# Performance work log

Hardware: AMD Instinct MI355X
Metric: run time of the kernel (lower is better)

Reference implementation:

```python
import jax, jax.numpy as jnp
import numpy as np

G = 8  # order of C8 rotation group

def expand_circulant(w):
    # w: [out_fields, in_fields, G] free params of a C8 regular->regular 1x1 conv.
    # Full weight: W[of*G+go, if*G+gi] = w[of, if, (go-gi) mod G]
    g = jnp.arange(G)
    idx = (g[:, None] - g[None, :]) % G            # [go, gi]
    Wf = w[:, :, idx]                              # [of, if, go, gi]
    Wf = jnp.transpose(Wf, (0, 2, 1, 3))           # [of, go, if, gi]
    return Wf.reshape(w.shape[0] * G, w.shape[1] * G)

def eq_proj(x2, w, b):
    # x2: [B, in_fields*G]; equivariant 1x1 conv = GEMM with circulant-expanded weight
    Wf = expand_circulant(w)                       # [out_fields*G, in_fields*G]
    bf = jnp.repeat(b, G)                          # per-field bias, shared across group dim
    return x2 @ Wf.T + bf

def setup_inputs() -> dict:
    key = jax.random.key(0)
    ks = jax.random.split(key, 12)
    B, d_model, n_head, d_k, d_v = 8192, 128, 8, 64, 64
    C = d_model * G                                # 1024
    s_in = 0.02
    inp = {
        'q': jax.random.normal(ks[0], (B, C, 1, 1), jnp.float32),
        'k': jax.random.normal(ks[1], (B, C, 1, 1), jnp.float32),
        'v': jax.random.normal(ks[2], (B, C, 1, 1), jnp.float32),
        'w_q': jax.random.normal(ks[3], (n_head * d_k, d_model, G), jnp.float32) * s_in,
        'b_q': jnp.zeros((n_head * d_k,), jnp.float32),
        'w_k': jax.random.normal(ks[4], (n_head * d_k, d_model, G), jnp.float32) * s_in,
        'b_k': jnp.zeros((n_head * d_k,), jnp.float32),
        'w_v': jax.random.normal(ks[5], (n_head * d_v, d_model, G), jnp.float32) * s_in,
        'b_v': jnp.zeros((n_head * d_v,), jnp.float32),
        'w_fc': jax.random.normal(ks[6], (d_model, n_head * d_v, G), jnp.float32) * s_in,
        'b_fc': jnp.zeros((d_model,), jnp.float32),
    }
    return inp

def reference(q, k, v, w_q, b_q, w_k, b_k, w_v, b_v, w_fc, b_fc):
    B, C = q.shape[0], q.shape[1]
    n_head, d_k = 8, 64
    d_v = 64
    temp = jnp.asarray(d_k ** 0.5, q.dtype)
    residual = q                                   # [B, C, 1, 1]
    q2 = q.reshape(B, C)
    k2 = k.reshape(B, C)
    v2 = v.reshape(B, C)
    # equivariant 1x1 conv projections -> [B, n_head*d_k*G]
    qp = eq_proj(q2, w_q, b_q).reshape(B, G, n_head, d_k).transpose(0, 2, 1, 3)  # [B,H,G,dk]
    kp = eq_proj(k2, w_k, b_k).reshape(B, G, n_head, d_k).transpose(0, 2, 1, 3)
    vp = eq_proj(v2, w_v, b_v).reshape(B, G, n_head, d_v).transpose(0, 2, 1, 3)
    # scaled dot-product attention over the G=8 group/orientation positions
    attn = jax.nn.softmax(jnp.einsum('bhqd,bhkd->bhqk', qp / temp, kp), axis=-1)  # [B,H,G,G]
    out = jnp.einsum('bhqk,bhkd->bhqd', attn, vp)  # [B,H,G,dv]
    # transpose(1,2) then flatten, exactly as torch .view(sz_b, -1, 1, 1)
    out = out.transpose(0, 2, 1, 3).reshape(B, G * n_head * d_v)
    out = eq_proj(out, w_fc, b_fc)                 # [B, d_model*G]
    out = out.reshape(B, C, 1, 1) + residual
    return out, attn
```

## Files before the change

kernel.cpp:

```cpp
#include <hip/hip_runtime.h>
#include <hip/hip_bf16.h>

typedef unsigned short u16;
typedef unsigned int u32;
typedef __bf16 bf16x8_t __attribute__((ext_vector_type(8)));
typedef float f32x4_t __attribute__((ext_vector_type(4)));

#define BK 64

__device__ __forceinline__ float b2f(u16 v) {
  return __uint_as_float(((u32)v) << 16);
}
__device__ __forceinline__ u16 f2b(float f) {
  __hip_bfloat16 h = __float2bfloat16(f);
  return *reinterpret_cast<u16*>(&h);
}
__device__ __forceinline__ float blo(u32 u) { return __uint_as_float(u << 16); }
__device__ __forceinline__ float bhi(u32 u) { return __uint_as_float(u & 0xffff0000u); }

__device__ __forceinline__ void async_lds16(const u16* g, u16* l) {
  __builtin_amdgcn_global_load_lds(
      (__attribute__((address_space(1))) void*)g,
      (__attribute__((address_space(3))) void*)l, 16, 0, 0);
}

__device__ __forceinline__ void expand8(const float* __restrict__ w,
                                        u16* __restrict__ dst, int I,
                                        int kshift, int gid) {
  const int n = gid >> kshift;
  const int kc = (gid & ((1 << kshift) - 1)) * 8;
  const int K = 8 << kshift;
  const float* wp = w + (size_t)((n >> 3) * I + (kc >> 3)) * 8;
  float4 w0 = *(const float4*)wp;
  float4 w1 = *(const float4*)(wp + 4);
  float w8[8] = {w0.x, w0.y, w0.z, w0.w, w1.x, w1.y, w1.z, w1.w};
  u16 t[8];
  const int r = (n - kc) & 7;
#pragma unroll
  for (int j = 0; j < 8; ++j) t[j] = f2b(w8[(r - j) & 7]);
  *(uint4*)(dst + (size_t)n * K + kc) = *(const uint4*)t;
}

__device__ __forceinline__ void cvt8(const float* __restrict__ src,
                                     u16* __restrict__ dst, int gid) {
  const float* p = src + (size_t)gid * 8;
  float4 a = *(const float4*)p;
  float4 b = *(const float4*)(p + 4);
  u16 t[8] = {f2b(a.x), f2b(a.y), f2b(a.z), f2b(a.w),
              f2b(b.x), f2b(b.y), f2b(b.z), f2b(b.w)};
  *(uint4*)(dst + (size_t)gid * 8) = *(const uint4*)t;
}

__global__ __launch_bounds__(256) void expand_all(
    const float* __restrict__ w_q, const float* __restrict__ w_k,
    const float* __restrict__ w_v, const float* __restrict__ w_fc,
    const float* __restrict__ q, const float* __restrict__ k,
    const float* __restrict__ v, u16* __restrict__ Wq, u16* __restrict__ Wk,
    u16* __restrict__ Wv, u16* __restrict__ Wfc, u16* __restrict__ qb,
    u16* __restrict__ kb, u16* __restrict__ vb, int cblocks) {
  const int e = blockIdx.x;
  if (e < 8192) {
    const int plane = e >> 11;
    const int gid = (e & 2047) * 256 + threadIdx.x;
    if (plane == 0) expand8(w_q, Wq, 128, 7, gid);
    else if (plane == 1) expand8(w_k, Wk, 128, 7, gid);
    else if (plane == 2) expand8(w_v, Wv, 128, 7, gid);
    else expand8(w_fc, Wfc, 512, 9, gid);
  } else {
    const int ce = e - 8192;
    const int plane = ce / cblocks;
    const int gid = (ce - plane * cblocks) * 256 + threadIdx.x;
    if (plane == 0) cvt8(q, qb, gid);
    else if (plane == 1) cvt8(k, kb, gid);
    else cvt8(v, vb, gid);
  }
}

__global__ __launch_bounds__(512, 2) void gemm_qkv8p(
    const u16* __restrict__ X0, const u16* __restrict__ X1,
    const u16* __restrict__ X2, const u16* __restrict__ W0,
    const u16* __restrict__ W1, const u16* __restrict__ W2,
    const float* __restrict__ b0v, const float* __restrict__ b1v,
    const float* __restrict__ b2v, u16* __restrict__ Y0, u16* __restrict__ Y1,
    u16* __restrict__ Y2, int M, int N, int K) {
  __shared__ __align__(16) u16 lds[65536];
  const int z = blockIdx.y;
  const u16* X = (z == 0) ? X0 : (z == 1) ? X1 : X2;
  const u16* W = (z == 0) ? W0 : (z == 1) ? W1 : W2;
  const float* bias = (z == 0) ? b0v : (z == 1) ? b1v : b2v;
  u16* Y = (z == 0) ? Y0 : (z == 1) ? Y1 : Y2;

  const int tid = threadIdx.x;
  const int bid = blockIdx.x;
  const int grid_m = M >> 8, grid_n = N >> 8;
  const int nb = grid_m * grid_n;
  int pid = (bid & 7) * (nb >> 3) + (bid >> 3);
  const int nig = 8 * grid_n;
  const int group_id = pid / nig;
  const int first_m = group_id * 8;
  const int gsz = min(8, grid_m - first_m);
  const int mt = first_m + (pid % gsz);
  const int ntile = (pid % nig) / gsz;
  const int m0 = mt << 8, n0 = ntile << 8;

  const int lane = tid & 63, wave = tid >> 6;
  const int wg = wave >> 2;
  const int wq = wave & 3;
  const int l16 = lane & 15, quad = lane >> 4;
  const int lswz = l16 & 7;

  const u16* gA = X + (size_t)m0 * K;
  const u16* gB = W + (size_t)n0 * K;
  const int srow = tid >> 3;
  const int skbg = (tid & 7) ^ (srow & 7);

  f32x4_t acc[8][4] = {};
  const int KT = K >> 6;
  const int niter = KT >> 1;

  auto stg = [&](int kt, int h, bool isB) {
    u16* l = lds + (isB ? 32768 : 0) + ((kt & 1) * 2 + h) * 8192 + tid * 8;
    const u16* g = (isB ? gB : gA) + (size_t)(h * 128 + srow) * K + kt * 64 +
                   skbg * 8;
    async_lds16(g, l);
    async_lds16(g + (size_t)64 * K, l + 4096);
  };
  auto ldA = [&](int kt, int mh, bf16x8_t (&a)[8]) {
    const u16* base = lds + ((kt & 1) * 2 + wg) * 8192 + (mh * 64 + l16) * 64;
#pragma unroll
    for (int mi = 0; mi < 4; ++mi)
#pragma unroll
      for (int ks = 0; ks < 2; ++ks)
        a[mi * 2 + ks] = *(const bf16x8_t*)(base + mi * 1024 +
                                            (((ks * 4 + quad) ^ lswz) * 8));
  };
  auto ldB = [&](int kt, int nh, bf16x8_t (&b)[4]) {
    const u16* base = lds + 32768 + ((kt & 1) * 2 + (wq >> 1)) * 8192 +
                      ((wq & 1) * 64 + nh * 32 + l16) * 64;
#pragma unroll
    for (int ni = 0; ni < 2; ++ni)
#pragma unroll
      for (int ks = 0; ks < 2; ++ks)
        b[ni * 2 + ks] = *(const bf16x8_t*)(base + ni * 1024 +
                                            (((ks * 4 + quad) ^ lswz) * 8));
  };
  auto mm = [&](int mh, int nh, bf16x8_t (&a)[8], bf16x8_t (&b)[4]) {
    __builtin_amdgcn_s_setprio(1);
#pragma unroll
    for (int mi = 0; mi < 4; ++mi)
#pragma unroll
      for (int ni = 0; ni < 2; ++ni)
#pragma unroll
        for (int ks = 0; ks < 2; ++ks)
          acc[mh * 4 + mi][nh * 2 + ni] = __builtin_amdgcn_mfma_f32_16x16x32_bf16(
              a[mi * 2 + ks], b[ni * 2 + ks], acc[mh * 4 + mi][nh * 2 + ni], 0,
              0, 0);
    __builtin_amdgcn_s_setprio(0);
  };
  auto bar = [] { __builtin_amdgcn_s_barrier(); };
  auto lgkm0 = [] {
    asm volatile("s_waitcnt lgkmcnt(0)" ::: "memory");
    __builtin_amdgcn_sched_barrier(0);
  };
  auto sched = [] { __builtin_amdgcn_sched_barrier(0); };

  bf16x8_t a0[8], a1[8], b0[4], b1[4];

  stg(0, 0, false); sched();
  stg(0, 0, true);  sched();
  stg(0, 1, false); sched();
  stg(0, 1, true);  sched();
  stg(1, 0, true);  sched();
  stg(1, 0, false); sched();
  asm volatile("s_waitcnt vmcnt(4)" ::: "memory");
  bar();
  sched();

  for (int it = 0; it < niter; ++it) {
    const int t = it * 2;
    const bool more = (t + 2 < KT);
    ldA(t, 0, a0); ldB(t, 0, b0);
    stg(t + 1, 1, false);
    sched(); bar(); lgkm0();
    mm(0, 0, a0, b0);
    bar();
    ldB(t, 1, b1);
    stg(t + 1, 1, true);
    sched(); bar(); lgkm0();
    mm(0, 1, a0, b1);
    bar();
    ldA(t, 1, a1);
    if (more) stg(t + 2, 0, true);
    sched(); bar(); lgkm0();
    mm(1, 1, a1, b1);
    bar();
    if (more) stg(t + 2, 0, false);
    sched();
    if (more) asm volatile("s_waitcnt vmcnt(4)" ::: "memory");
    else      asm volatile("s_waitcnt vmcnt(0)" ::: "memory");
    bar(); lgkm0();
    mm(1, 0, a1, b0);
    bar();
    ldA(t + 1, 0, a0); ldB(t + 1, 0, b0);
    if (more) stg(t + 2, 1, false);
    sched(); bar(); lgkm0();
    mm(0, 0, a0, b0);
    bar();
    ldB(t + 1, 1, b1);
    if (more) stg(t + 2, 1, true);
    sched(); bar(); lgkm0();
    mm(0, 1, a0, b1);
    bar();
    ldA(t + 1, 1, a1);
    if (more) stg(t + 3, 0, true);
    sched(); bar(); lgkm0();
    mm(1, 1, a1, b1);
    bar();
    if (more) {
      stg(t + 3, 0, false);
      sched();
      asm volatile("s_waitcnt vmcnt(4)" ::: "memory");
      bar(); lgkm0();
      mm(1, 0, a1, b0);
      bar();
    } else {
      lgkm0();
      mm(1, 0, a1, b0);
    }
  }

#pragma unroll
  for (int mi = 0; mi < 8; ++mi) {
#pragma unroll
    for (int r = 0; r < 4; ++r) {
      const int rw = m0 + wg * 128 + mi * 16 + quad * 4 + r;
      u32 h0, h1, h2, h3;
      {
        const int cb = n0 + wq * 64 + l16;
        h0 = (u32)f2b(acc[mi][0][r] + bias[(cb) >> 3]);
        h1 = (u32)f2b(acc[mi][1][r] + bias[(cb + 16) >> 3]);
        h2 = (u32)f2b(acc[mi][2][r] + bias[(cb + 32) >> 3]);
        h3 = (u32)f2b(acc[mi][3][r] + bias[(cb + 48) >> 3]);
      }
      const int s0 = quad * 16 + 4 * (l16 & 3);
      u32 g0[4], g1[4], g2[4], g3[4];
#pragma unroll
      for (int j = 0; j < 4; ++j) {
        g0[j] = (u32)__shfl((int)h0, s0 + j);
        g1[j] = (u32)__shfl((int)h1, s0 + j);
        g2[j] = (u32)__shfl((int)h2, s0 + j);
        g3[j] = (u32)__shfl((int)h3, s0 + j);
      }
      const int myni = l16 >> 2;
      u32 a_[4];
#pragma unroll
      for (int j = 0; j < 4; ++j) {
        u32 s01 = (myni & 1) ? g1[j] : g0[j];
        u32 s23 = (myni & 1) ? g3[j] : g2[j];
        a_[j] = (myni & 2) ? s23 : s01;
      }
      uint2 wv;
      wv.x = a_[0] | (a_[1] << 16);
      wv.y = a_[2] | (a_[3] << 16);
      *(uint2*)&Y[(size_t)rw * N + n0 + wq * 64 + 4 * l16] = wv;
    }
  }
}

__global__ __launch_bounds__(256) void gemm_fc2(
    const u16* __restrict__ Aa, const u16* __restrict__ Ab,
    const u16* __restrict__ W, const float* __restrict__ bias,
    const float* __restrict__ res, float* __restrict__ Y, int M, int N, int K,
    int halfM) {
  constexpr int TN = 128;
  __shared__ __align__(16) u16 As[128 * BK];
  __shared__ __align__(16) u16 Bs[TN * BK];
  const int tid = threadIdx.x;
  const int bid = blockIdx.x;

  const int grid_m = M >> 7, grid_n = N / TN;
  const int nb = grid_m * grid_n;
  int pid = (bid & 7) * (nb >> 3) + (bid >> 3);
  const int nig = 8 * grid_n;
  const int group_id = pid / nig;
  const int first_m = group_id * 8;
  const int gsz = min(8, grid_m - first_m);
  const int mt = first_m + (pid % gsz);
  const int nt = (pid % nig) / gsz;
  const int m0 = mt << 7, n0 = nt * TN;

  const u16* Xb = (m0 < halfM) ? Aa : Ab;
  const int m0l = (m0 < halfM) ? m0 : m0 - halfM;

  const int lane = tid & 63;
  const int wave = tid >> 6;
  const int wm = (wave >> 1) * 64;
  const int wn = (wave & 1) * (TN / 2);
  const int l16 = lane & 15;
  const int quad = lane >> 4;
  constexpr int NJ = TN >> 5;

  f32x4_t acc[4][NJ] = {};

  const int row0 = tid >> 3;
  const int kgl = ((tid & 7) ^ (row0 & 7)) * 8;

  for (int k0 = 0; k0 < K; k0 += BK) {
#pragma unroll
    for (int it = 0; it < TN / 32; ++it)
      async_lds16(W + (size_t)(n0 + row0 + it * 32) * K + (k0 + kgl),
                  &Bs[(tid + it * 256) * 8]);
#pragma unroll
    for (int it = 0; it < 4; ++it)
      async_lds16(Xb + (size_t)(m0l + row0 + it * 32) * K + (k0 + kgl),
                  &As[(tid + it * 256) * 8]);
    __syncthreads();
#pragma unroll
    for (int half = 0; half < 2; ++half) {
      bf16x8_t af[4], bfr[NJ];
#pragma unroll
      for (int i = 0; i < 4; ++i)
        af[i] = *(const bf16x8_t*)&As[(wm + i * 16 + l16) * BK +
                                      (((quad + half * 4) ^ (l16 & 7)) * 8)];
#pragma unroll
      for (int j = 0; j < NJ; ++j)
        bfr[j] = *(const bf16x8_t*)&Bs[(wn + j * 16 + l16) * BK +
                                       (((quad + half * 4) ^ (l16 & 7)) * 8)];
#pragma unroll
      for (int i = 0; i < 4; ++i)
#pragma unroll
        for (int j = 0; j < NJ; ++j)
          acc[i][j] =
              __builtin_amdgcn_mfma_f32_16x16x32_bf16(af[i], bfr[j], acc[i][j], 0, 0, 0);
    }
    __syncthreads();
  }

#pragma unroll
  for (int i = 0; i < 4; ++i) {
#pragma unroll
    for (int r = 0; r < 4; ++r) {
      const int rw = m0 + wm + i * 16 + quad * 4 + r;
#pragma unroll
      for (int j = 0; j < NJ; ++j) {
        const int col = n0 + wn + j * 16 + l16;
        float vv = acc[i][j][r] + bias[col >> 3] + res[(size_t)rw * N + col];
        Y[(size_t)rw * N + col] = vv;
      }
    }
  }
}

__global__ __launch_bounds__(256) void attn_kernel(
    const u16* __restrict__ qp, const u16* __restrict__ kp, const u16* vp,
    float* __restrict__ probs, u16* o, int iters) {
  __shared__ __align__(16) u16 Qs[4][8 * 72];
  __shared__ __align__(16) u16 Ks[4][8 * 72];
  __shared__ __align__(16) u16 Vs[4][512];
  __shared__ __align__(16) float Ps[4][64];
  const int tid = threadIdx.x;
  const int wave = tid >> 6;
  const int lane = tid & 63;
  const int r = lane >> 3, c = lane & 7;
  const int ls = r * 72 + c * 8;
  const int qg = r;
  const int kg = c;

  auto pairof = [&](int it) { return (it * gridDim.x + blockIdx.x) * 4 + wave; };
  auto gaddr = [&](int it) {
    const int pr = pairof(it);
    return (size_t)(pr >> 3) * 4096 + (size_t)r * 512 + (pr & 7) * 64 + c * 8;
  };
  auto vaddr = [&](int it) {
    const int pr = pairof(it);
    return (size_t)(pr >> 3) * 4096 + (size_t)(lane >> 3) * 512 +
           (pr & 7) * 64 + (lane & 7) * 8;
  };

  uint4 qr = *(const uint4*)(qp + gaddr(0));
  uint4 kr = *(const uint4*)(kp + gaddr(0));
  uint4 vr = *(const uint4*)(vp + vaddr(0));

  for (int it = 0; it < iters; ++it) {
    *(uint4*)&Qs[wave][ls] = qr;
    *(uint4*)&Ks[wave][ls] = kr;
    *(uint4*)&Vs[wave][lane * 8] = vr;
    const int pair = pairof(it);
    const int b = pair >> 3;
    const int h = pair & 7;
    if (it + 1 < iters) {
      qr = *(const uint4*)(qp + gaddr(it + 1));
      kr = *(const uint4*)(kp + gaddr(it + 1));
      vr = *(const uint4*)(vp + vaddr(it + 1));
    }
    float s = 0.f;
#pragma unroll
    for (int d8 = 0; d8 < 8; ++d8) {
      uint4 qa = *(const uint4*)&Qs[wave][qg * 72 + d8 * 8];
      uint4 ka = *(const uint4*)&Ks[wave][kg * 72 + d8 * 8];
      s += blo(qa.x) * blo(ka.x) + bhi(qa.x) * bhi(ka.x);
      s += blo(qa.y) * blo(ka.y) + bhi(qa.y) * bhi(ka.y);
      s += blo(qa.z) * blo(ka.z) + bhi(qa.z) * bhi(ka.z);
      s += blo(qa.w) * blo(ka.w) + bhi(qa.w) * bhi(ka.w);
    }
    s *= 0.125f;
    float mx = s;
    mx = fmaxf(mx, __shfl_xor(mx, 1));
    mx = fmaxf(mx, __shfl_xor(mx, 2));
    mx = fmaxf(mx, __shfl_xor(mx, 4));
    float e = __expf(s - mx);
    float sum = e;
    sum += __shfl_xor(sum, 1);
    sum += __shfl_xor(sum, 2);
    sum += __shfl_xor(sum, 4);
    const float p = e / sum;
    probs[(size_t)pair * 64 + lane] = p;
    Ps[wave][lane] = p;
    float vcf[8];
#pragma unroll
    for (int k2 = 0; k2 < 8; ++k2)
      vcf[k2] = b2f(Vs[wave][k2 * 64 + lane]);
#pragma unroll
    for (int q2 = 0; q2 < 8; ++q2) {
      float4 p0 = *(const float4*)&Ps[wave][q2 * 8];
      float4 p1 = *(const float4*)&Ps[wave][q2 * 8 + 4];
      float acc = p0.x * vcf[0] + p0.y * vcf[1] + p0.z * vcf[2] + p0.w * vcf[3] +
                  p1.x * vcf[4] + p1.y * vcf[5] + p1.z * vcf[6] + p1.w * vcf[7];
      o[(size_t)b * 4096 + q2 * 512 + h * 64 + lane] = f2b(acc);
    }
  }
}

extern "C" void kernel_launch(void* const* d_in, const int* in_sizes, int n_in,
                              void* d_out, int out_size, void* d_ws, size_t ws_size,
                              hipStream_t stream) {
  const float* q = (const float*)d_in[0];
  const float* k = (const float*)d_in[1];
  const float* v = (const float*)d_in[2];
  const float* w_q = (const float*)d_in[3];
  const float* b_q = (const float*)d_in[4];
  const float* w_k = (const float*)d_in[5];
  const float* b_k = (const float*)d_in[6];
  const float* w_v = (const float*)d_in[7];
  const float* b_v = (const float*)d_in[8];
  const float* w_fc = (const float*)d_in[9];
  const float* b_fc = (const float*)d_in[10];

  const int B = in_sizes[0] / 1024;
  float* out = (float*)d_out;
  float* probs = out + (size_t)B * 1024;

  u16* Wq = (u16*)d_ws;
  u16* Wk = Wq + (size_t)4096 * 1024;
  u16* Wv = Wk + (size_t)4096 * 1024;
  u16* Wfc = Wv + (size_t)4096 * 1024;
  u16* qb = Wfc + (size_t)4096 * 1024;
  u16* kb = qb + (size_t)B * 1024;
  u16* vb = kb + (size_t)B * 1024;
  u16* scratch = vb + (size_t)B * 1024;
  const size_t fixed_bytes =
      ((size_t)4 * 4096 * 1024 + (size_t)3 * B * 1024) * sizeof(u16);

  const size_t per_row = (size_t)(4 * 4096) * sizeof(u16);
  int chunkB = 256;
  for (int c = B; c >= 256; c >>= 1) {
    if (fixed_bytes + (size_t)c * per_row <= ws_size) { chunkB = c; break; }
  }

  u16* qp = scratch;
  u16* kp = qp + (size_t)chunkB * 4096;
  u16* vp = kp + (size_t)chunkB * 4096;
  u16* ao0 = vp + (size_t)chunkB * 4096;

  const int cblocks = B / 2;
  expand_all<<<8192 + 3 * cblocks, 256, 0, stream>>>(
      w_q, w_k, w_v, w_fc, q, k, v, Wq, Wk, Wv, Wfc, qb, kb, vb, cblocks);

  const bool two_chunks = (chunkB * 2 == B);
  for (int cs = 0; cs < B; cs += chunkB) {
    const int nb_p = (chunkB / 256) * (4096 / 256);
    gemm_qkv8p<<<dim3(nb_p, 3), 512, 0, stream>>>(
        qb + (size_t)cs * 1024, kb + (size_t)cs * 1024, vb + (size_t)cs * 1024,
        Wq, Wk, Wv, b_q, b_k, b_v, qp, kp, vp, chunkB, 4096, 1024);
    const int ablocks = (chunkB >= 1024) ? 2048 : chunkB * 2;
    const int aiters = (chunkB * 8) / (ablocks * 4);
    u16* aoc = (cs == 0) ? ao0 : vp;
    attn_kernel<<<ablocks, 256, 0, stream>>>(qp, kp, vp,
                                             probs + (size_t)cs * 512, aoc,
                                             aiters);
    if (!two_chunks) {
      const int nb_fc = (chunkB / 128) * (1024 / 128);
      gemm_fc2<<<nb_fc, 256, 0, stream>>>(aoc, aoc, Wfc, b_fc,
                                          q + (size_t)cs * 1024,
                                          out + (size_t)cs * 1024, chunkB, 1024,
                                          4096, chunkB);
    }
  }
  if (two_chunks) {
    const int nb_fc = (B / 128) * (1024 / 128);
    gemm_fc2<<<nb_fc, 256, 0, stream>>>(ao0, vp, Wfc, b_fc, q, out, B, 1024,
                                        4096, chunkB);
  }
}
```

Baseline: 570.2 us.

## Add 8-wave 256x128 pipelined FC GEMM kernel for two-chunk path

Adds a new output-projection GEMM kernel with 512 threads, 256x128 tiles, and double-buffered async global-to-LDS loads interleaved with MFMA phases using barriers and priority hints. It replaces the 256-thread 128x128 fc kernel when the batch is split into two chunks. The aim is better operand reuse per block and overlap of memory loads with matrix math. In exchange it needs large LDS (96KB) and half as many blocks, which may reduce occupancy or tail balance.

```diff
diff --git a/kernel.cpp b/kernel.cpp
--- a/kernel.cpp
+++ b/kernel.cpp
@@ -267,6 +267,177 @@
   }
 }
 
+__global__ __launch_bounds__(512, 2) void gemm_fc8p(
+    const u16* __restrict__ Aa, const u16* __restrict__ Ab,
+    const u16* __restrict__ W, const float* __restrict__ bias,
+    const float* __restrict__ res, float* __restrict__ Y, int M, int N, int K,
+    int halfM) {
+  __shared__ __align__(16) u16 lds[49152];
+  const int tid = threadIdx.x;
+  const int bid = blockIdx.x;
+  const int grid_m = M >> 8, grid_n = N >> 7;
+  const int nb = grid_m * grid_n;
+  int pid = (bid & 7) * (nb >> 3) + (bid >> 3);
+  const int nig = 8 * grid_n;
+  const int group_id = pid / nig;
+  const int first_m = group_id * 8;
+  const int gsz = min(8, grid_m - first_m);
+  const int mt = first_m + (pid % gsz);
+  const int ntile = (pid % nig) / gsz;
+  const int m0 = mt << 8, n0 = ntile << 7;
+
+  const u16* Xb = (m0 < halfM) ? Aa : Ab;
+  const int m0l = (m0 < halfM) ? m0 : m0 - halfM;
+
+  const int lane = tid & 63, wave = tid >> 6;
+  const int wg = wave >> 2;
+  const int wq = wave & 3;
+  const int l16 = lane & 15, quad = lane >> 4;
+  const int lswz = l16 & 7;
+
+  const u16* gA = Xb + (size_t)m0l * K;
+  const u16* gB = W + (size_t)n0 * K;
+  const int srow = tid >> 3;
+  const int skbg = (tid & 7) ^ (srow & 7);
+
+  f32x4_t acc[8][2] = {};
+  const int KT = K >> 6;
+  const int niter = KT >> 1;
+
+  auto stgA = [&](int kt, int h) {
+    u16* l = lds + ((kt & 1) * 2 + h) * 8192 + tid * 8;
+    const u16* g = gA + (size_t)(h * 128 + srow) * K + kt * 64 + skbg * 8;
+    async_lds16(g, l);
+    async_lds16(g + (size_t)64 * K, l + 4096);
+  };
+  auto stgB = [&](int kt, int h) {
+    u16* l = lds + 32768 + ((kt & 1) * 2 + h) * 4096 + tid * 8;
+    const u16* g = gB + (size_t)(h * 64 + srow) * K + kt * 64 + skbg * 8;
+    async_lds16(g, l);
+  };
+  auto ldA = [&](int kt, int mh, bf16x8_t (&a)[8]) {
+    const u16* base = lds + ((kt & 1) * 2 + wg) * 8192 + (mh * 64 + l16) * 64;
+#pragma unroll
+    for (int mi = 0; mi < 4; ++mi)
+#pragma unroll
+      for (int ks = 0; ks < 2; ++ks)
+        a[mi * 2 + ks] = *(const bf16x8_t*)(base + mi * 1024 +
+                                            (((ks * 4 + quad) ^ lswz) * 8));
+  };
+  auto ldB = [&](int kt, int nh, bf16x8_t (&b)[2]) {
+    const u16* base = lds + 32768 + ((kt & 1) * 2 + (wq >> 1)) * 4096 +
+                      ((wq & 1) * 32 + nh * 16 + l16) * 64;
+#pragma unroll
+    for (int ks = 0; ks < 2; ++ks)
+      b[ks] = *(const bf16x8_t*)(base + (((ks * 4 + quad) ^ lswz) * 8));
+  };
+  auto mm = [&](int mh, int nh, bf16x8_t (&a)[8], bf16x8_t (&b)[2]) {
+    __builtin_amdgcn_s_setprio(1);
+#pragma unroll
+    for (int mi = 0; mi < 4; ++mi)
+#pragma unroll
+      for (int ks = 0; ks < 2; ++ks)
+        acc[mh * 4 + mi][nh] = __builtin_amdgcn_mfma_f32_16x16x32_bf16(
+            a[mi * 2 + ks], b[ks], acc[mh * 4 + mi][nh], 0, 0, 0);
+    __builtin_amdgcn_s_setprio(0);
+  };
+  auto bar = [] { __builtin_amdgcn_s_barrier(); };
+  auto lgkm0 = [] {
+    asm volatile("s_waitcnt lgkmcnt(0)" ::: "memory");
+    __builtin_amdgcn_sched_barrier(0);
+  };
+  auto sched = [] { __builtin_amdgcn_sched_barrier(0); };
+
+  bf16x8_t a0[8], a1[8], b0[2], b1[2];
+
+  stgA(0, 0); sched();
+  stgB(0, 0); sched();
+  stgA(0, 1); sched();
+  stgB(0, 1); sched();
+  stgB(1, 0); sched();
+  stgA(1, 0); sched();
+  asm volatile("s_waitcnt vmcnt(3)" ::: "memory");
+  bar();
+  sched();
+
+  for (int it = 0; it < niter; ++it) {
+    const int t = it * 2;
+    const bool more = (t + 2 < KT);
+    ldA(t, 0, a0); ldB(t, 0, b0);
+    stgA(t + 1, 1);
+    sched(); bar(); lgkm0();
+    mm(0, 0, a0, b0);
+    bar();
+    ldB(t, 1, b1);
+    stgB(t + 1, 1);
+    sched(); bar(); lgkm0();
+    mm(0, 1, a0, b1);
+    bar();
+    ldA(t, 1, a1);
+    if (more) stgB(t + 2, 0);
+    sched(); bar(); lgkm0();
+    mm(1, 1, a1, b1);
+    bar();
+    if (more) stgA(t + 2, 0);
+    sched();
+    if (more) asm volatile("s_waitcnt vmcnt(3)" ::: "memory");
+    else      asm volatile("s_waitcnt vmcnt(0)" ::: "memory");
+    bar(); lgkm0();
+    mm(1, 0, a1, b0);
+    bar();
+    ldA(t + 1, 0, a0); ldB(t + 1, 0, b0);
+    if (more) stgA(t + 2, 1);
+    sched(); bar(); lgkm0();
+    mm(0, 0, a0, b0);
+    bar();
+    ldB(t + 1, 1, b1);
+    if (more) stgB(t + 2, 1);
+    sched(); bar(); lgkm0();
+    mm(0, 1, a0, b1);
+    bar();
+    ldA(t + 1, 1, a1);
+    if (more) stgB(t + 3, 0);
+    sched(); bar(); lgkm0();
+    mm(1, 1, a1, b1);
+    bar();
+    if (more) {
+      stgA(t + 3, 0);
+      sched();
+      asm volatile("s_waitcnt vmcnt(3)" ::: "memory");
+      bar(); lgkm0();
+      mm(1, 0, a1, b0);
+      bar();
+    } else {
+      lgkm0();
+      mm(1, 0, a1, b0);
+    }
+  }
+
+#pragma unroll
+  for (int mi = 0; mi < 8; ++mi) {
+#pragma unroll
+    for (int r = 0; r < 4; ++r) {
+      const int rw = m0 + wg * 128 + mi * 16 + quad * 4 + r;
+      const float h0 = acc[mi][0][r];
+      const float h1 = acc[mi][1][r];
+      const int c0 = 2 * l16, c1 = 2 * l16 + 1;
+      const int ls0 = quad * 16 + (c0 & 15);
+      const int ls1 = quad * 16 + (c1 & 15);
+      float s00 = __shfl(h0, ls0), s01 = __shfl(h1, ls0);
+      float s10 = __shfl(h0, ls1), s11 = __shfl(h1, ls1);
+      float v0 = (c0 & 16) ? s01 : s00;
+      float v1 = (c1 & 16) ? s11 : s10;
+      const int col0 = n0 + wq * 32 + c0;
+      const size_t base = (size_t)rw * N + col0;
+      float2 rr = *(const float2*)&res[base];
+      v0 += bias[col0 >> 3] + rr.x;
+      v1 += bias[(col0 + 1) >> 3] + rr.y;
+      float2 wv; wv.x = v0; wv.y = v1;
+      *(float2*)&Y[base] = wv;
+    }
+  }
+}
+
 __global__ __launch_bounds__(256) void gemm_fc2(
     const u16* __restrict__ Aa, const u16* __restrict__ Ab,
     const u16* __restrict__ W, const float* __restrict__ bias,
@@ -497,8 +668,8 @@
     }
   }
   if (two_chunks) {
-    const int nb_fc = (B / 128) * (1024 / 128);
-    gemm_fc2<<<nb_fc, 256, 0, stream>>>(ao0, vp, Wfc, b_fc, q, out, B, 1024,
-                                        4096, chunkB);
-  }
-}
+    const int nb_fc = (B / 256) * (1024 / 128);
+    gemm_fc8p<<<nb_fc, 512, 0, stream>>>(ao0, vp, Wfc, b_fc, q, out, B, 1024,
+                                         4096, chunkB);
+  }
+}
```

Result: faster. 548.0 us (-3.9%).
